# Kernel tuning notes

Measured on AMD Instinct MI355X. Metric: run time of the kernel, lower is better.

The kernel has to match this reference:

```python
import jax, jax.numpy as jnp
import numpy as np

EMB_DIM = 300
TEMPERATURE = 0.01
REWEIGHT = True
N = 8192
NUM_GROUPS = 100


def setup_inputs() -> dict:
    key = jax.random.key(0)
    ks = jax.random.split(key, 6)
    s = 1.0 / np.sqrt(EMB_DIM)
    x = jax.random.normal(ks[0], (N, EMB_DIM), dtype=jnp.float32)
    W1 = jax.random.normal(ks[1], (EMB_DIM, EMB_DIM), dtype=jnp.float32) * s
    b1 = jnp.zeros((EMB_DIM,), dtype=jnp.float32)
    W2 = jax.random.normal(ks[2], (EMB_DIM, EMB_DIM), dtype=jnp.float32) * s
    b2 = jnp.zeros((EMB_DIM,), dtype=jnp.float32)
    # labels in [1, 100]: all > 0 so the group_y>0 filter keeps every row
    labels = jax.random.randint(ks[3], (N,), 1, NUM_GROUPS + 1, dtype=jnp.int32)
    return {"x": x, "W1": W1, "b1": b1, "W2": W2, "b2": b2, "labels": labels}


def reference(x, W1, b1, W2, b2, labels):
    # projector: Linear -> ReLU -> Linear
    h = jax.nn.relu(x @ W1 + b1) @ W2 + b2
    # L2 normalize rows
    f = h / jnp.linalg.norm(h, axis=1, keepdims=True)
    # pairwise similarity / temperature, row-max subtracted (detached)
    logits = (f @ f.T) / TEMPERATURE                      # [N, N]
    logits = logits - jax.lax.stop_gradient(jnp.max(logits, axis=1, keepdims=True))

    lab = labels[:, None]
    mask = (lab == lab.T).astype(logits.dtype)            # same-group mask
    logits_mask = 1.0 - jnp.eye(mask.shape[0], dtype=logits.dtype)  # drop diagonal
    mask = mask * logits_mask

    # rows with at least one positive (torch filters these; we weight instead)
    pos_count = jnp.sum(mask, axis=1)                     # [N]
    valid = pos_count > 0

    if REWEIGHT:
        pos_m = logits_mask * mask
        neg_m = logits_mask * (1.0 - mask)
        pos_sum = jnp.sum(pos_m, axis=1, keepdims=True)
        neg_sum = jnp.sum(neg_m, axis=1, keepdims=True)
        log_pos = jnp.where(pos_sum > 0, jnp.log(jnp.maximum(pos_sum, 1.0)), 0.0)
        log_neg = jnp.where(neg_sum > 0, jnp.log(jnp.maximum(neg_sum, 1.0)), 0.0)
        logits = (logits - log_pos) * pos_m + (logits - log_neg) * neg_m

    exp_logits = jnp.exp(logits) * logits_mask
    log_prob = logits - jnp.log(jnp.sum(exp_logits, axis=1, keepdims=True))
    mean_log_prob_pos = jnp.sum(mask * log_prob, axis=1) / jnp.where(valid, pos_count, 1.0)
    validf = valid.astype(logits.dtype)
    loss = -TEMPERATURE * jnp.sum(mean_log_prob_pos * validf) / jnp.sum(validf)
    return loss
```

## Files before the change

kernel.cpp:

```cpp
#include <hip/hip_runtime.h>
#include <hip/hip_bf16.h>


#define N_ROWS 8192
#define D_PAD 320
#define NG 100
#define TEMP 0.01f
#define NSPLIT 32
#define JCHUNK (N_ROWS / NSPLIT)
#define LOG2E100 144.2695041f

typedef short short8v __attribute__((ext_vector_type(8)));
typedef float float4v __attribute__((ext_vector_type(4)));

__device__ __forceinline__ short f2bf(float f) {
  union { __hip_bfloat16 h; short s; } u;
  u.h = __float2bfloat16(f);
  return u.s;
}

__global__ __launch_bounds__(256) void setup_kernel(
    const float* __restrict__ W1, const float* __restrict__ W2,
    const int* __restrict__ labels,
    __hip_bfloat16* __restrict__ w1t, __hip_bfloat16* __restrict__ w2t,
    int* __restrict__ counts32)
{
  __shared__ float T[64][65];
  __shared__ int hc[NG + 1];
  int b = blockIdx.x, tid = threadIdx.x;
  if (b < 50) {
    int isW2 = b >= 25;
    int t5 = isW2 ? b - 25 : b;
    int k0 = (t5 / 5) * 64, n0 = (t5 % 5) * 64;
    const float* W = isW2 ? W2 : W1;
    __hip_bfloat16* dst = isW2 ? w2t : w1t;
#pragma unroll
    for (int t = 0; t < 16; ++t) {
      int e = tid + t * 256;
      int r = e >> 6, c = e & 63;
      T[r][c] = (k0 + r < 300 && n0 + c < 300)
                  ? W[(size_t)(k0 + r) * 300 + (n0 + c)] : 0.0f;
    }
    __syncthreads();
#pragma unroll
    for (int t = 0; t < 16; ++t) {
      int e = tid + t * 256;
      int nn = e >> 6, kk = e & 63;
      dst[(size_t)(n0 + nn) * D_PAD + (k0 + kk)] = __float2bfloat16(T[kk][nn]);
    }
  } else {
    int h = b - 50;
    if (tid <= NG) hc[tid] = 0;
    __syncthreads();
    atomicAdd(&hc[labels[h * 256 + tid]], 1);
    __syncthreads();
    if (tid <= NG) counts32[h * (NG + 1) + tid] = hc[tid];
  }
}

__global__ __launch_bounds__(256, 2) void mlp_fused_kernel(
    const float* __restrict__ x, const __hip_bfloat16* __restrict__ w1t,
    const __hip_bfloat16* __restrict__ w2t, const float* __restrict__ b1,
    const float* __restrict__ b2, __hip_bfloat16* __restrict__ fb)
{
  __shared__ __align__(16) short H1[16 * D_PAD];
  __shared__ float ssq_s[16];
  const short* W1s = (const short*)w1t;
  const short* W2s = (const short*)w2t;
  int tid = threadIdx.x;
  int lane = tid & 63, p = tid >> 6;
  int g = lane >> 4, lc = lane & 15, sw = lc & 7;
  int i0 = blockIdx.x * 16;

  if (tid < 16) ssq_s[tid] = 0.f;

  short8v afr[10];
  {
    const float* xp = x + (size_t)(i0 + lc) * 300;
#pragma unroll
    for (int kk = 0; kk < 10; ++kk) {
      int k0 = kk * 32 + g * 8;
      short8v v;
      if (k0 + 8 <= 300) {
        float4 a = *(const float4*)(xp + k0);
        float4 c = *(const float4*)(xp + k0 + 4);
        v[0] = f2bf(a.x); v[1] = f2bf(a.y); v[2] = f2bf(a.z); v[3] = f2bf(a.w);
        v[4] = f2bf(c.x); v[5] = f2bf(c.y); v[6] = f2bf(c.z); v[7] = f2bf(c.w);
      } else if (k0 < 300) {
        float4 a = *(const float4*)(xp + k0);
        v[0] = f2bf(a.x); v[1] = f2bf(a.y); v[2] = f2bf(a.z); v[3] = f2bf(a.w);
        v[4] = 0; v[5] = 0; v[6] = 0; v[7] = 0;
      } else {
        v = short8v{0, 0, 0, 0, 0, 0, 0, 0};
      }
      afr[kk] = v;
    }
  }

  for (int nt = 0; nt < 5; ++nt) {
    int n = (p * 5 + nt) * 16 + lc;
    float4v acc = {0.f, 0.f, 0.f, 0.f};
    const short* wp = W1s + (size_t)n * D_PAD + g * 8;
#pragma unroll
    for (int kk = 0; kk < 10; ++kk) {
      short8v bf = *(const short8v*)(wp + kk * 32);
      acc = __builtin_amdgcn_mfma_f32_16x16x32_bf16(afr[kk], bf, acc, 0, 0, 0);
    }
    float bv = (n < 300) ? b1[n] : 0.0f;
    int q = n >> 3;
#pragma unroll
    for (int r = 0; r < 4; ++r) {
      int row = g * 4 + r;
      H1[row * D_PAD + ((q ^ (row & 7)) << 3) + (n & 7)] =
          f2bf(fmaxf(acc[r] + bv, 0.0f));
    }
  }
  __syncthreads();

  short8v hfr[10];
  {
    const short* rp = H1 + lc * D_PAD;
#pragma unroll
    for (int kk = 0; kk < 10; ++kk)
      hfr[kk] = *(const short8v*)(rp + (((g + 4 * kk) ^ sw) << 3));
  }

  float4v h2a[5];
  for (int nt = 0; nt < 5; ++nt) {
    int n = (p * 5 + nt) * 16 + lc;
    float4v acc = {0.f, 0.f, 0.f, 0.f};
    const short* wp = W2s + (size_t)n * D_PAD + g * 8;
#pragma unroll
    for (int kk = 0; kk < 10; ++kk) {
      short8v bf = *(const short8v*)(wp + kk * 32);
      acc = __builtin_amdgcn_mfma_f32_16x16x32_bf16(hfr[kk], bf, acc, 0, 0, 0);
    }
    float bv = (n < 300) ? b2[n] : 0.0f;
#pragma unroll
    for (int r = 0; r < 4; ++r) acc[r] += bv;
    h2a[nt] = acc;
  }

  float ss[4] = {0.f, 0.f, 0.f, 0.f};
#pragma unroll
  for (int nt = 0; nt < 5; ++nt)
#pragma unroll
    for (int r = 0; r < 4; ++r) ss[r] = fmaf(h2a[nt][r], h2a[nt][r], ss[r]);
  for (int m = 1; m < 16; m <<= 1)
#pragma unroll
    for (int r = 0; r < 4; ++r) ss[r] += __shfl_xor(ss[r], m, 64);
  if (lc == 0)
#pragma unroll
    for (int r = 0; r < 4; ++r) atomicAdd(&ssq_s[g * 4 + r], ss[r]);
  __syncthreads();
  float inv[4];
#pragma unroll
  for (int r = 0; r < 4; ++r) inv[r] = rsqrtf(ssq_s[g * 4 + r]);
#pragma unroll
  for (int nt = 0; nt < 5; ++nt) {
    int n = (p * 5 + nt) * 16 + lc;
#pragma unroll
    for (int r = 0; r < 4; ++r) {
      int row = i0 + g * 4 + r;
      fb[(size_t)row * D_PAD + n] = __float2bfloat16(h2a[nt][r] * inv[r]);
    }
  }
}

__global__ __launch_bounds__(256) void group_kernel(
    const __hip_bfloat16* __restrict__ Fb, const int* __restrict__ labels,
    float* __restrict__ sPar, float* __restrict__ sAar)
{
  __shared__ __align__(16) short Bs[64 * D_PAD];
  __shared__ int memb[256];
  __shared__ int cnt;
  const short* Fs = (const short*)Fb;
  int tid = threadIdx.x;
  int lane = tid & 63, wave = tid >> 6;
  int g = lane >> 4, lc = lane & 15, sw = lc & 7;
  int grp = blockIdx.x + 1;
  if (tid == 0) cnt = 0;
  __syncthreads();
  for (int i = tid; i < N_ROWS; i += 256)
    if (labels[i] == grp) { int p = atomicAdd(&cnt, 1); if (p < 256) memb[p] = i; }
  __syncthreads();
  int c = cnt > 256 ? 256 : cnt;
  int nt = (c + 63) >> 6;
  for (int it = 0; it < nt; ++it) {
    short8v afr[10];
    {
      int islot = it * 64 + wave * 16 + lc;
      int arow = memb[islot < c ? islot : 0];
      const short* ap = Fs + (size_t)arow * D_PAD + g * 8;
#pragma unroll
      for (int kk = 0; kk < 10; ++kk) afr[kk] = *(const short8v*)(ap + kk * 32);
    }
    int iglobr[4]; bool ivalid[4];
    for (int r = 0; r < 4; ++r) {
      int islot = it * 64 + wave * 16 + g * 4 + r;
      ivalid[r] = islot < c;
      iglobr[r] = memb[islot < c ? islot : 0];
    }
    float sp[4] = {}, sa[4] = {};
    for (int jt = 0; jt < nt; ++jt) {
      __syncthreads();
      {
        const int4* src = (const int4*)Fs;
        int4* dst = (int4*)Bs;
#pragma unroll
        for (int t = 0; t < 10; ++t) {
          int e = tid + t * 256;
          int r = e / 40, q = e - r * 40;
          int jslot = jt * 64 + r;
          int grow = memb[jslot < c ? jslot : 0];
          dst[r * 40 + (q ^ (r & 7))] = src[(size_t)grow * 40 + q];
        }
      }
      __syncthreads();
      for (int js = 0; js < 4; ++js) {
        float4v acc = {0.f, 0.f, 0.f, 0.f};
        const short* rowp = Bs + (js * 16 + lc) * D_PAD;
#pragma unroll
        for (int kk = 0; kk < 10; ++kk) {
          short8v bf = *(const short8v*)(rowp + (((g + 4 * kk) ^ sw) << 3));
          acc = __builtin_amdgcn_mfma_f32_16x16x32_bf16(afr[kk], bf, acc, 0, 0, 0);
        }
        int jslot = jt * 64 + js * 16 + lc;
        bool jv = jslot < c;
        int jglob = memb[jslot < c ? jslot : 0];
#pragma unroll
        for (int r = 0; r < 4; ++r) {
          float a = acc[r];
          float e = exp2f(fmaf(a, LOG2E100, -LOG2E100));
          bool ok = jv && ivalid[r] && (jglob != iglobr[r]);
          sp[r] += ok ? e : 0.f;
          sa[r] += ok ? a : 0.f;
        }
      }
    }
    for (int m = 1; m < 16; m <<= 1)
      for (int r = 0; r < 4; ++r) {
        sp[r] += __shfl_xor(sp[r], m, 64);
        sa[r] += __shfl_xor(sa[r], m, 64);
      }
    if (lc == 0)
      for (int r = 0; r < 4; ++r)
        if (ivalid[r]) { sPar[iglobr[r]] = sp[r]; sAar[iglobr[r]] = sa[r]; }
  }
}

__global__ __launch_bounds__(256, 2) void pairwise_kernel(
    const __hip_bfloat16* __restrict__ Fb, float* __restrict__ partE)
{
  __shared__ __align__(16) short Bs[64 * D_PAD];
  const short* Fs = (const short*)Fb;
  int tid = threadIdx.x;
  int lane = tid & 63, wave = tid >> 6;
  int g = lane >> 4, lc = lane & 15, sw = lc & 7;
  int i0 = blockIdx.x * 128;
  int split = blockIdx.y;
  int jstart = split * JCHUNK;

  short8v afr[2][10];
  for (int s = 0; s < 2; ++s) {
    const short* ap = Fs + (size_t)(i0 + s * 64 + wave * 16 + lc) * D_PAD + g * 8;
#pragma unroll
    for (int kk = 0; kk < 10; ++kk) afr[s][kk] = *(const short8v*)(ap + kk * 32);
  }
  float sE[2][4] = {};

  for (int jt = 0; jt < JCHUNK / 64; ++jt) {
    int jb = jstart + jt * 64;
    __syncthreads();
    {
      const int4* src = (const int4*)Fs;
#pragma unroll
      for (int t = 0; t < 10; ++t) {
        int e = tid + t * 256;
        int r = e / 40, q = e - r * 40;
        int qs = q ^ (r & 7);
        __builtin_amdgcn_global_load_lds(
            (const __attribute__((address_space(1))) void*)(src + (size_t)(jb + r) * 40 + qs),
            (__attribute__((address_space(3))) void*)((int4*)Bs + e),
            16, 0, 0);
      }
    }
    __syncthreads();
    for (int js = 0; js < 4; ++js) {
      float4v acc0 = {0.f, 0.f, 0.f, 0.f}, acc1 = {0.f, 0.f, 0.f, 0.f};
      const short* rowp = Bs + (js * 16 + lc) * D_PAD;
#pragma unroll
      for (int kk = 0; kk < 10; ++kk) {
        short8v bf = *(const short8v*)(rowp + (((g + 4 * kk) ^ sw) << 3));
        acc0 = __builtin_amdgcn_mfma_f32_16x16x32_bf16(afr[0][kk], bf, acc0, 0, 0, 0);
        acc1 = __builtin_amdgcn_mfma_f32_16x16x32_bf16(afr[1][kk], bf, acc1, 0, 0, 0);
      }
#pragma unroll
      for (int s = 0; s < 2; ++s) {
        float4v acc = s ? acc1 : acc0;
        bool dt = (jb == i0 + s * 64) && (js == wave);
#pragma unroll
        for (int r = 0; r < 4; ++r) {
          float e = exp2f(fmaf(acc[r], LOG2E100, -LOG2E100));
          if (dt && lc == g * 4 + r) e = 0.0f;
          sE[s][r] += e;
        }
      }
    }
  }
  for (int m = 1; m < 16; m <<= 1)
#pragma unroll
    for (int s = 0; s < 2; ++s)
#pragma unroll
      for (int r = 0; r < 4; ++r) sE[s][r] += __shfl_xor(sE[s][r], m, 64);
  if (lc == 0)
    for (int s = 0; s < 2; ++s)
      for (int r = 0; r < 4; ++r)
        partE[split * N_ROWS + i0 + s * 64 + wave * 16 + g * 4 + r] = sE[s][r];
}

__global__ __launch_bounds__(256) void final_a_kernel(
    const float* __restrict__ partE, const float* __restrict__ sPar,
    const float* __restrict__ sAar, const int* __restrict__ counts32,
    const int* __restrict__ labels, float* __restrict__ blk)
{
  __shared__ int cnt_s[NG + 1];
  __shared__ float rm[256], rv[256];
  int tid = threadIdx.x;
  int i = blockIdx.x * 256 + tid;
  if (tid <= NG) {
    int c = 0;
    for (int s = 0; s < 32; ++s) c += counts32[s * (NG + 1) + tid];
    cnt_s[tid] = c;
  }
  float sE = 0.f;
  for (int s = 0; s < NSPLIT; ++s) sE += partE[s * N_ROWS + i];
  __syncthreads();
  float M = 0.f, V = 0.f;
  int pc = cnt_s[labels[i]] - 1;
  if (pc > 0) {
    float P = sPar[i], A = sAar[i];
    float Q = sE - P;
    float pcf = (float)pc, ncf = (float)(N_ROWS - 1 - pc);
    float Z = P / pcf + Q / ncf;
    M = 100.0f * A / pcf - 100.0f - logf(pcf) - logf(Z);
    V = 1.f;
  }
  rm[tid] = M; rv[tid] = V;
  __syncthreads();
  for (int s2 = 128; s2 > 0; s2 >>= 1) {
    if (tid < s2) { rm[tid] += rm[tid + s2]; rv[tid] += rv[tid + s2]; }
    __syncthreads();
  }
  if (tid == 0) { blk[blockIdx.x] = rm[0]; blk[32 + blockIdx.x] = rv[0]; }
}

__global__ void final_b_kernel(const float* __restrict__ blk, float* __restrict__ out)
{
  int lane = threadIdx.x;
  float m = (lane < 32) ? blk[lane] : 0.f;
  float v = (lane < 32) ? blk[32 + lane] : 0.f;
  for (int s = 1; s < 32; s <<= 1) { m += __shfl_xor(m, s, 64); v += __shfl_xor(v, s, 64); }
  if (lane == 0) out[0] = (v > 0.f) ? (-TEMP * m / v) : 0.f;
}

extern "C" void kernel_launch(void* const* d_in, const int* in_sizes, int n_in,
                              void* d_out, int out_size, void* d_ws, size_t ws_size,
                              hipStream_t stream)
{
  const float* x  = (const float*)d_in[0];
  const float* W1 = (const float*)d_in[1];
  const float* b1 = (const float*)d_in[2];
  const float* W2 = (const float*)d_in[3];
  const float* b2 = (const float*)d_in[4];
  const int* labels = (const int*)d_in[5];

  char* ws = (char*)d_ws;
  __hip_bfloat16* fb    = (__hip_bfloat16*)(ws);
  __hip_bfloat16* w1t   = (__hip_bfloat16*)(ws + 5242880);
  __hip_bfloat16* w2t   = (__hip_bfloat16*)(ws + 5447680);
  int*         counts32 = (int*)(ws + 5652480);
  float*        partE   = (float*)(ws + 5665536);
  float*        sPar    = (float*)(ws + 6714112);
  float*        sAar    = (float*)(ws + 6746880);
  float*        blk     = (float*)(ws + 6779648);

  setup_kernel<<<82, 256, 0, stream>>>(W1, W2, labels, w1t, w2t, counts32);
  mlp_fused_kernel<<<512, 256, 0, stream>>>(x, w1t, w2t, b1, b2, fb);
  group_kernel<<<NG, 256, 0, stream>>>(fb, labels, sPar, sAar);
  pairwise_kernel<<<dim3(64, NSPLIT), 256, 0, stream>>>(fb, partE);
  final_a_kernel<<<32, 256, 0, stream>>>(partE, sPar, sAar, counts32, labels, blk);
  final_b_kernel<<<1, 64, 0, stream>>>(blk, (float*)d_out);
}
```

Baseline: 182.2 us.

## Store normalized features in FP8 and use FP8 MFMA for similarity GEMMs

The normalized feature matrix is now written as 8-bit FP8 instead of bf16. The group and pairwise kernels switch to the fp8 16x16x32 MFMA with 8-byte operands and a padded, unswizzled LDS layout, and global_load_lds is replaced with register copies. The group kernel now builds its member list with a wave ballot instead of shared atomics, and splits row tiles across two blocks per group. The pairwise inner loop branches off the diagonal-tile masking. This halves feature bandwidth and raises MFMA throughput, but with temperature 0.01 the FP8 rounding of similarities is multiplied by 100 before the exponential, so accuracy of the loss is at serious risk.

```diff
diff --git a/kernel.cpp b/kernel.cpp
--- a/kernel.cpp
+++ b/kernel.cpp
@@ -3,12 +3,13 @@
 
 
 #define N_ROWS 8192
-#define D_PAD 320
 #define NG 100
 #define TEMP 0.01f
 #define NSPLIT 32
 #define JCHUNK (N_ROWS / NSPLIT)
 #define LOG2E100 144.2695041f
+#define FB_STRIDE 320
+#define LDS_STRIDE 336
 
 typedef short short8v __attribute__((ext_vector_type(8)));
 typedef float float4v __attribute__((ext_vector_type(4)));
@@ -46,7 +47,7 @@
     for (int t = 0; t < 16; ++t) {
       int e = tid + t * 256;
       int nn = e >> 6, kk = e & 63;
-      dst[(size_t)(n0 + nn) * D_PAD + (k0 + kk)] = __float2bfloat16(T[kk][nn]);
+      dst[(size_t)(n0 + nn) * 320 + (k0 + kk)] = __float2bfloat16(T[kk][nn]);
     }
   } else {
     int h = b - 50;
@@ -61,9 +62,9 @@
 __global__ __launch_bounds__(256, 2) void mlp_fused_kernel(
     const float* __restrict__ x, const __hip_bfloat16* __restrict__ w1t,
     const __hip_bfloat16* __restrict__ w2t, const float* __restrict__ b1,
-    const float* __restrict__ b2, __hip_bfloat16* __restrict__ fb)
-{
-  __shared__ __align__(16) short H1[16 * D_PAD];
+    const float* __restrict__ b2, unsigned char* __restrict__ fb)
+{
+  __shared__ __align__(16) short H1[16 * 320];
   __shared__ float ssq_s[16];
   const short* W1s = (const short*)w1t;
   const short* W2s = (const short*)w2t;
@@ -100,7 +101,7 @@
   for (int nt = 0; nt < 5; ++nt) {
     int n = (p * 5 + nt) * 16 + lc;
     float4v acc = {0.f, 0.f, 0.f, 0.f};
-    const short* wp = W1s + (size_t)n * D_PAD + g * 8;
+    const short* wp = W1s + (size_t)n * 320 + g * 8;
 #pragma unroll
     for (int kk = 0; kk < 10; ++kk) {
       short8v bf = *(const short8v*)(wp + kk * 32);
@@ -111,7 +112,7 @@
 #pragma unroll
     for (int r = 0; r < 4; ++r) {
       int row = g * 4 + r;
-      H1[row * D_PAD + ((q ^ (row & 7)) << 3) + (n & 7)] =
+      H1[row * 320 + ((q ^ (row & 7)) << 3) + (n & 7)] =
           f2bf(fmaxf(acc[r] + bv, 0.0f));
     }
   }
@@ -119,7 +120,7 @@
 
   short8v hfr[10];
   {
-    const short* rp = H1 + lc * D_PAD;
+    const short* rp = H1 + lc * 320;
 #pragma unroll
     for (int kk = 0; kk < 10; ++kk)
       hfr[kk] = *(const short8v*)(rp + (((g + 4 * kk) ^ sw) << 3));
@@ -129,7 +130,7 @@
   for (int nt = 0; nt < 5; ++nt) {
     int n = (p * 5 + nt) * 16 + lc;
     float4v acc = {0.f, 0.f, 0.f, 0.f};
-    const short* wp = W2s + (size_t)n * D_PAD + g * 8;
+    const short* wp = W2s + (size_t)n * 320 + g * 8;
 #pragma unroll
     for (int kk = 0; kk < 10; ++kk) {
       short8v bf = *(const short8v*)(wp + kk * 32);
@@ -162,38 +163,54 @@
 #pragma unroll
     for (int r = 0; r < 4; ++r) {
       int row = i0 + g * 4 + r;
-      fb[(size_t)row * D_PAD + n] = __float2bfloat16(h2a[nt][r] * inv[r]);
+      float v = h2a[nt][r] * inv[r];
+      int pk = __builtin_amdgcn_cvt_pk_fp8_f32(v, v, 0, false);
+      fb[(size_t)row * FB_STRIDE + n] = (unsigned char)(pk & 0xFF);
     }
   }
 }
 
 __global__ __launch_bounds__(256) void group_kernel(
-    const __hip_bfloat16* __restrict__ Fb, const int* __restrict__ labels,
+    const unsigned char* __restrict__ Fb, const int* __restrict__ labels,
     float* __restrict__ sPar, float* __restrict__ sAar)
 {
-  __shared__ __align__(16) short Bs[64 * D_PAD];
+  __shared__ __align__(16) unsigned char Bs[64 * LDS_STRIDE];
   __shared__ int memb[256];
   __shared__ int cnt;
-  const short* Fs = (const short*)Fb;
   int tid = threadIdx.x;
   int lane = tid & 63, wave = tid >> 6;
-  int g = lane >> 4, lc = lane & 15, sw = lc & 7;
+  int g = lane >> 4, lc = lane & 15;
   int grp = blockIdx.x + 1;
-  if (tid == 0) cnt = 0;
+
+  if (wave == 0) {
+    int base = 0;
+    for (int t = 0; t < 32; ++t) {
+      int4 L = ((const int4*)labels)[t * 64 + lane];
+      int rb = (t * 64 + lane) * 4;
+      int comp[4] = {L.x, L.y, L.z, L.w};
+#pragma unroll
+      for (int c4 = 0; c4 < 4; ++c4) {
+        unsigned long long m = __ballot(comp[c4] == grp);
+        if (comp[c4] == grp) {
+          int pp = base + __popcll(m & ((1ull << lane) - 1ull));
+          if (pp < 256) memb[pp] = rb + c4;
+        }
+        base += __popcll(m);
+      }
+    }
+    if (lane == 0) cnt = base > 256 ? 256 : base;
+  }
   __syncthreads();
-  for (int i = tid; i < N_ROWS; i += 256)
-    if (labels[i] == grp) { int p = atomicAdd(&cnt, 1); if (p < 256) memb[p] = i; }
-  __syncthreads();
-  int c = cnt > 256 ? 256 : cnt;
+  int c = cnt;
   int nt = (c + 63) >> 6;
-  for (int it = 0; it < nt; ++it) {
-    short8v afr[10];
+  for (int it = blockIdx.y; it < nt; it += 2) {
+    long afr[10];
     {
       int islot = it * 64 + wave * 16 + lc;
       int arow = memb[islot < c ? islot : 0];
-      const short* ap = Fs + (size_t)arow * D_PAD + g * 8;
-#pragma unroll
-      for (int kk = 0; kk < 10; ++kk) afr[kk] = *(const short8v*)(ap + kk * 32);
+      const unsigned char* ap = Fb + (size_t)arow * FB_STRIDE + g * 8;
+#pragma unroll
+      for (int kk = 0; kk < 10; ++kk) afr[kk] = *(const long*)(ap + kk * 32);
     }
     int iglobr[4]; bool ivalid[4];
     for (int r = 0; r < 4; ++r) {
@@ -205,25 +222,25 @@
     for (int jt = 0; jt < nt; ++jt) {
       __syncthreads();
       {
-        const int4* src = (const int4*)Fs;
+        const int4* src = (const int4*)Fb;
         int4* dst = (int4*)Bs;
 #pragma unroll
-        for (int t = 0; t < 10; ++t) {
+        for (int t = 0; t < 5; ++t) {
           int e = tid + t * 256;
-          int r = e / 40, q = e - r * 40;
+          int r = e / 20, q = e - r * 20;
           int jslot = jt * 64 + r;
           int grow = memb[jslot < c ? jslot : 0];
-          dst[r * 40 + (q ^ (r & 7))] = src[(size_t)grow * 40 + q];
+          dst[r * 21 + q] = src[(size_t)grow * 20 + q];
         }
       }
       __syncthreads();
       for (int js = 0; js < 4; ++js) {
         float4v acc = {0.f, 0.f, 0.f, 0.f};
-        const short* rowp = Bs + (js * 16 + lc) * D_PAD;
+        const unsigned char* rowp = Bs + (js * 16 + lc) * LDS_STRIDE + g * 8;
 #pragma unroll
         for (int kk = 0; kk < 10; ++kk) {
-          short8v bf = *(const short8v*)(rowp + (((g + 4 * kk) ^ sw) << 3));
-          acc = __builtin_amdgcn_mfma_f32_16x16x32_bf16(afr[kk], bf, acc, 0, 0, 0);
+          long bv = *(const long*)(rowp + kk * 32);
+          acc = __builtin_amdgcn_mfma_f32_16x16x32_fp8_fp8(afr[kk], bv, acc, 0, 0, 0);
         }
         int jslot = jt * 64 + js * 16 + lc;
         bool jv = jslot < c;
@@ -250,22 +267,22 @@
 }
 
 __global__ __launch_bounds__(256, 2) void pairwise_kernel(
-    const __hip_bfloat16* __restrict__ Fb, float* __restrict__ partE)
-{
-  __shared__ __align__(16) short Bs[64 * D_PAD];
-  const short* Fs = (const short*)Fb;
+    const unsigned char* __restrict__ Fb, float* __restrict__ partE)
+{
+  __shared__ __align__(16) unsigned char Bs[64 * LDS_STRIDE];
   int tid = threadIdx.x;
   int lane = tid & 63, wave = tid >> 6;
-  int g = lane >> 4, lc = lane & 15, sw = lc & 7;
+  int g = lane >> 4, lc = lane & 15;
   int i0 = blockIdx.x * 128;
   int split = blockIdx.y;
   int jstart = split * JCHUNK;
 
-  short8v afr[2][10];
+  long afr[2][10];
   for (int s = 0; s < 2; ++s) {
-    const short* ap = Fs + (size_t)(i0 + s * 64 + wave * 16 + lc) * D_PAD + g * 8;
-#pragma unroll
-    for (int kk = 0; kk < 10; ++kk) afr[s][kk] = *(const short8v*)(ap + kk * 32);
+    const unsigned char* ap =
+        Fb + (size_t)(i0 + s * 64 + wave * 16 + lc) * FB_STRIDE + g * 8;
+#pragma unroll
+    for (int kk = 0; kk < 10; ++kk) afr[s][kk] = *(const long*)(ap + kk * 32);
   }
   float sE[2][4] = {};
 
@@ -273,37 +290,40 @@
     int jb = jstart + jt * 64;
     __syncthreads();
     {
-      const int4* src = (const int4*)Fs;
-#pragma unroll
-      for (int t = 0; t < 10; ++t) {
+      const int4* src = (const int4*)Fb;
+      int4* dst = (int4*)Bs;
+#pragma unroll
+      for (int t = 0; t < 5; ++t) {
         int e = tid + t * 256;
-        int r = e / 40, q = e - r * 40;
-        int qs = q ^ (r & 7);
-        __builtin_amdgcn_global_load_lds(
-            (const __attribute__((address_space(1))) void*)(src + (size_t)(jb + r) * 40 + qs),
-            (__attribute__((address_space(3))) void*)((int4*)Bs + e),
-            16, 0, 0);
+        int r = e / 20, q = e - r * 20;
+        dst[r * 21 + q] = src[(size_t)(jb + r) * 20 + q];
       }
     }
     __syncthreads();
     for (int js = 0; js < 4; ++js) {
       float4v acc0 = {0.f, 0.f, 0.f, 0.f}, acc1 = {0.f, 0.f, 0.f, 0.f};
-      const short* rowp = Bs + (js * 16 + lc) * D_PAD;
+      const unsigned char* rowp = Bs + (js * 16 + lc) * LDS_STRIDE + g * 8;
 #pragma unroll
       for (int kk = 0; kk < 10; ++kk) {
-        short8v bf = *(const short8v*)(rowp + (((g + 4 * kk) ^ sw) << 3));
-        acc0 = __builtin_amdgcn_mfma_f32_16x16x32_bf16(afr[0][kk], bf, acc0, 0, 0, 0);
-        acc1 = __builtin_amdgcn_mfma_f32_16x16x32_bf16(afr[1][kk], bf, acc1, 0, 0, 0);
+        long bv = *(const long*)(rowp + kk * 32);
+        acc0 = __builtin_amdgcn_mfma_f32_16x16x32_fp8_fp8(afr[0][kk], bv, acc0, 0, 0, 0);
+        acc1 = __builtin_amdgcn_mfma_f32_16x16x32_fp8_fp8(afr[1][kk], bv, acc1, 0, 0, 0);
       }
 #pragma unroll
       for (int s = 0; s < 2; ++s) {
         float4v acc = s ? acc1 : acc0;
         bool dt = (jb == i0 + s * 64) && (js == wave);
-#pragma unroll
-        for (int r = 0; r < 4; ++r) {
-          float e = exp2f(fmaf(acc[r], LOG2E100, -LOG2E100));
-          if (dt && lc == g * 4 + r) e = 0.0f;
-          sE[s][r] += e;
+        if (dt) {
+#pragma unroll
+          for (int r = 0; r < 4; ++r) {
+            float e = exp2f(fmaf(acc[r], LOG2E100, -LOG2E100));
+            if (lc == g * 4 + r) e = 0.0f;
+            sE[s][r] += e;
+          }
+        } else {
+#pragma unroll
+          for (int r = 0; r < 4; ++r)
+            sE[s][r] += exp2f(fmaf(acc[r], LOG2E100, -LOG2E100));
         }
       }
     }
@@ -376,18 +396,18 @@
   const int* labels = (const int*)d_in[5];
 
   char* ws = (char*)d_ws;
-  __hip_bfloat16* fb    = (__hip_bfloat16*)(ws);
-  __hip_bfloat16* w1t   = (__hip_bfloat16*)(ws + 5242880);
-  __hip_bfloat16* w2t   = (__hip_bfloat16*)(ws + 5447680);
-  int*         counts32 = (int*)(ws + 5652480);
-  float*        partE   = (float*)(ws + 5665536);
-  float*        sPar    = (float*)(ws + 6714112);
-  float*        sAar    = (float*)(ws + 6746880);
-  float*        blk     = (float*)(ws + 6779648);
+  unsigned char*  fb    = (unsigned char*)(ws);
+  __hip_bfloat16* w1t   = (__hip_bfloat16*)(ws + 2621440);
+  __hip_bfloat16* w2t   = (__hip_bfloat16*)(ws + 2826240);
+  int*         counts32 = (int*)(ws + 3031040);
+  float*        partE   = (float*)(ws + 3044096);
+  float*        sPar    = (float*)(ws + 4092672);
+  float*        sAar    = (float*)(ws + 4125440);
+  float*        blk     = (float*)(ws + 4158208);
 
   setup_kernel<<<82, 256, 0, stream>>>(W1, W2, labels, w1t, w2t, counts32);
   mlp_fused_kernel<<<512, 256, 0, stream>>>(x, w1t, w2t, b1, b2, fb);
-  group_kernel<<<NG, 256, 0, stream>>>(fb, labels, sPar, sAar);
+  group_kernel<<<dim3(NG, 2), 256, 0, stream>>>(fb, labels, sPar, sAar);
   pairwise_kernel<<<dim3(64, NSPLIT), 256, 0, stream>>>(fb, partE);
   final_a_kernel<<<32, 256, 0, stream>>>(partE, sPar, sAar, counts32, labels, blk);
   final_b_kernel<<<1, 64, 0, stream>>>(blk, (float*)d_out);
```

Measured after the change: 175.0 us. 1.04x faster.
